# Performance work log

Measured on AMD Instinct MI355X. Metric: run time of the kernel, lower is better.

The kernel has to match this reference:

```python
import jax, jax.numpy as jnp
import numpy as np

N, E, D = 20000, 160000, 128   # nodes, edges, d_model
GH, HC = 4, 128                # TransformerConv heads, per-head channels (= out_channels)
MH = 4                         # temporal MHA heads
MC = D // MH                   # temporal MHA per-head dim
EPS = 1e-5


def layer_norm(x, g, b):
    mu = x.mean(-1, keepdims=True)
    var = ((x - mu) ** 2).mean(-1, keepdims=True)
    return (x - mu) * jax.lax.rsqrt(var + EPS) * g + b


def forward(x, temporal_encoding, gq_w, gq_b, gk_w, gk_b, gv_w, gv_b, gs_w, gs_b,
            mha_wq, mha_bq, mha_wk, mha_bk, mha_wv, mha_bv, mha_wo, mha_bo,
            ffn_w1, ffn_b1, ffn_w2, ffn_b2,
            ln1_g, ln1_b, ln2_g, ln2_b, ln3_g, ln3_b, edge_index):
    src, dst = edge_index[0], edge_index[1]
    n = x.shape[0]
    # --- TransformerConv(in=D, out=D, heads=GH, concat=False, root_weight=True) ---
    q = (x @ gq_w.T + gq_b).reshape(n, GH, HC)
    k = (x @ gk_w.T + gk_b).reshape(n, GH, HC)
    v = (x @ gv_w.T + gv_b).reshape(n, GH, HC)
    # per-edge attention logits: <q_i, k_j> / sqrt(out_channels), message j->i
    alpha = (q[dst] * k[src]).sum(-1) / jnp.sqrt(jnp.asarray(HC, x.dtype))  # [E, GH]
    # numerically-stable segment softmax over incoming edges of each dst node
    m = jax.ops.segment_max(alpha, dst, num_segments=n)                     # [N, GH]
    ex = jnp.exp(alpha - m[dst])
    den = jax.ops.segment_sum(ex, dst, num_segments=n)
    w = ex / den[dst]                                                       # [E, GH]
    agg = jax.ops.segment_sum(w[..., None] * v[src], dst, num_segments=n)  # [N, GH, HC]
    graph_out = agg.mean(1) + (x @ gs_w.T + gs_b)  # concat=False -> head mean; + root skip lin
    x1 = layer_norm(x + graph_out, ln1_g, ln1_b)   # dropout is identity at eval
    # --- temporal MHA: per-node query (len 1) attends to its temporal encoding (kv len 1) ---
    tq = (x1 @ mha_wq.T + mha_bq).reshape(n, MH, MC)
    tk = (temporal_encoding @ mha_wk.T + mha_bk).reshape(n, MH, MC)
    tv = (temporal_encoding @ mha_wv.T + mha_bv).reshape(n, MH, MC)
    scores = (tq * tk).sum(-1, keepdims=True) / jnp.sqrt(jnp.asarray(MC, x.dtype))  # [N, MH, 1]
    attn = jax.nn.softmax(scores, axis=-1)  # exactly ones (single kv position); kept for fidelity
    temp_out = (attn * tv).reshape(n, D) @ mha_wo.T + mha_bo
    x2 = layer_norm(x1 + temp_out, ln2_g, ln2_b)
    # --- FFN ---
    h = jax.nn.relu(x2 @ ffn_w1.T + ffn_b1)
    ffn_out = h @ ffn_w2.T + ffn_b2
    return layer_norm(x2 + ffn_out, ln3_g, ln3_b)


def setup_inputs() -> dict:
    ks = jax.random.split(jax.random.key(0), 16)
    s = 0.05
    def p(i, shape):
        return jax.random.normal(ks[i], shape, jnp.float32) * s
    z = lambda *sh: jnp.zeros(sh, jnp.float32)
    o = lambda *sh: jnp.ones(sh, jnp.float32)
    return {
        "x": p(0, (N, D)),
        "temporal_encoding": p(1, (N, D)),
        "gq_w": p(2, (GH * HC, D)), "gq_b": z(GH * HC),
        "gk_w": p(3, (GH * HC, D)), "gk_b": z(GH * HC),
        "gv_w": p(4, (GH * HC, D)), "gv_b": z(GH * HC),
        "gs_w": p(5, (D, D)), "gs_b": z(D),
        "mha_wq": p(6, (D, D)), "mha_bq": z(D),
        "mha_wk": p(7, (D, D)), "mha_bk": z(D),
        "mha_wv": p(8, (D, D)), "mha_bv": z(D),
        "mha_wo": p(9, (D, D)), "mha_bo": z(D),
        "ffn_w1": p(10, (4 * D, D)), "ffn_b1": z(4 * D),
        "ffn_w2": p(11, (D, 4 * D)), "ffn_b2": z(D),
        "ln1_g": o(D), "ln1_b": z(D),
        "ln2_g": o(D), "ln2_b": z(D),
        "ln3_g": o(D), "ln3_b": z(D),
        "edge_index": jax.random.randint(ks[12], (2, E), 0, N, jnp.int32),
    }


def reference(x, temporal_encoding, gq_w, gq_b, gk_w, gk_b, gv_w, gv_b, gs_w, gs_b,
              mha_wq, mha_bq, mha_wk, mha_bk, mha_wv, mha_bv, mha_wo, mha_bo,
              ffn_w1, ffn_b1, ffn_w2, ffn_b2,
              ln1_g, ln1_b, ln2_g, ln2_b, ln3_g, ln3_b, edge_index):
    return forward(x, temporal_encoding, gq_w, gq_b, gk_w, gk_b, gv_w, gv_b, gs_w, gs_b,
                   mha_wq, mha_bq, mha_wk, mha_bk, mha_wv, mha_bv, mha_wo, mha_bo,
                   ffn_w1, ffn_b1, ffn_w2, ffn_b2,
                   ln1_g, ln1_b, ln2_g, ln2_b, ln3_g, ln3_b, edge_index)
```

## Files before the change

kernel.cpp:

```cpp
#include <hip/hip_runtime.h>

#define NN 20000
#define EE 160000
#define DD 128
#define GHC 512
#define INV_SQRT_HC 0.08838834764831845f

typedef __attribute__((ext_vector_type(8))) short short8;
typedef __attribute__((ext_vector_type(4))) short short4v;
typedef __attribute__((ext_vector_type(4))) float float4v;
typedef __attribute__((ext_vector_type(2))) float float2v;
typedef __attribute__((ext_vector_type(4))) unsigned uint4v;
typedef __attribute__((ext_vector_type(2))) unsigned uint2v;

__device__ inline float bf2f(unsigned short u) {
    union { unsigned u; float f; } x; x.u = ((unsigned)u) << 16; return x.f;
}
__device__ inline unsigned short f2bf(float f) {
    union { float f; unsigned u; } x; x.f = f;
    unsigned u = x.u;
    unsigned r = (u + 0x7fffu + ((u >> 16) & 1u)) >> 16;
    return (unsigned short)r;
}
__device__ inline unsigned cvt_pk_bf16(float a, float b) {
    unsigned d;
    asm("v_cvt_pk_bf16_f32 %0, %1, %2" : "=v"(d) : "v"(a), "v"(b));
    return d;
}

__device__ inline void stage16(const short8* gsrc, short8* ldst) {
    __builtin_amdgcn_global_load_lds(
        (const __attribute__((address_space(1))) void*)gsrc,
        (__attribute__((address_space(3))) void*)ldst, 16, 0, 0);
}

#if defined(__has_builtin)
#if __has_builtin(__builtin_amdgcn_cvt_pk_f32_fp8) && __has_builtin(__builtin_amdgcn_cvt_pk_fp8_f32)
#define HW_FP8 1
#endif
#endif
#ifndef HW_FP8
#define HW_FP8 0
#endif

#if !HW_FP8
__device__ inline unsigned char sw_enc_fp8(float f) {
    if (!(f == f)) return 0x7f;
    unsigned s = (f < 0.f) ? 0x80u : 0u;
    float a = fabsf(f);
    if (a >= 448.f) return (unsigned char)(s | 0x7e);
    if (a < 5.96046448e-8f) return (unsigned char)s;
    int e; frexpf(a, &e);
    int E = e - 1;
    if (E < -6) E = -6;
    float q = ldexpf(rintf(ldexpf(a, 3 - E)), E - 3);
    if (q == 0.f) return (unsigned char)s;
    union { float f; unsigned u; } x; x.f = q;
    int qe = (int)((x.u >> 23) & 0xff) - 127;
    if (qe < -6) {
        unsigned mant = (unsigned)rintf(ldexpf(q, 9));
        return (unsigned char)(s | mant);
    }
    unsigned mant = (x.u >> 20) & 7;
    int ebits = qe + 7;
    if (ebits > 15) { ebits = 15; mant = 6; }
    return (unsigned char)(s | ((unsigned)ebits << 3) | mant);
}
__device__ inline float sw_dec_fp8(unsigned char u) {
    unsigned s = u >> 7, e = (u >> 3) & 15, m = u & 7;
    float v = e ? ldexpf((float)(8 + m), (int)e - 10) : ldexpf((float)m, -9);
    return s ? -v : v;
}
#endif

__device__ inline unsigned fp8_enc4(float a, float b, float c, float d) {
#if HW_FP8
    int r = __builtin_amdgcn_cvt_pk_fp8_f32(a, b, 0, false);
    r = __builtin_amdgcn_cvt_pk_fp8_f32(c, d, r, true);
    return (unsigned)r;
#else
    return (unsigned)sw_enc_fp8(a) | ((unsigned)sw_enc_fp8(b) << 8)
         | ((unsigned)sw_enc_fp8(c) << 16) | ((unsigned)sw_enc_fp8(d) << 24);
#endif
}
__device__ inline float2v fp8_dec2_lo(unsigned w) {
#if HW_FP8
    return __builtin_amdgcn_cvt_pk_f32_fp8((int)w, false);
#else
    float2v r;
    r[0] = sw_dec_fp8((unsigned char)(w & 0xff));
    r[1] = sw_dec_fp8((unsigned char)((w >> 8) & 0xff));
    return r;
#endif
}
__device__ inline float2v fp8_dec2_hi(unsigned w) {
#if HW_FP8
    return __builtin_amdgcn_cvt_pk_f32_fp8((int)w, true);
#else
    float2v r;
    r[0] = sw_dec_fp8((unsigned char)((w >> 16) & 0xff));
    r[1] = sw_dec_fp8((unsigned char)(w >> 24));
    return r;
#endif
}

struct WPack { const void* in[18]; };
__device__ __constant__ const int WSZ[18] = {
    65536, 65536, 65536, 512, 512, 512,
    16384, 128, 65536, 512, 65536, 128,
    128, 128, 128, 128, 128, 128 };

__global__ void prep_kernel(const float* __restrict__ x, const float* __restrict__ te,
                            unsigned short* __restrict__ xcout, WPack p,
                            unsigned short* __restrict__ wcout,
                            const float* __restrict__ wv, const float* __restrict__ bv,
                            const float* __restrict__ wo, const float* __restrict__ bo,
                            unsigned short* __restrict__ wcomb,
                            unsigned short* __restrict__ bcomb,
                            const int* __restrict__ e_dst, int* __restrict__ counts)
{
    const int b = blockIdx.x;
    const int tid = threadIdx.x;
    if (b < 1024) {
        const long n4half = (long)NN * DD / 4;
        short4v* out4 = reinterpret_cast<short4v*>(xcout);
        long i = (long)b * 256 + tid;
        const long stride = 1024L * 256;
        const long tot = 2 * n4half;
        for (; i < tot; i += stride) {
            const float4v* src = (i < n4half)
                ? reinterpret_cast<const float4v*>(x)
                : reinterpret_cast<const float4v*>(te) - n4half;
            float4v v = src[i];
            short4v o;
            o[0] = (short)f2bf(v[0]); o[1] = (short)f2bf(v[1]);
            o[2] = (short)f2bf(v[2]); o[3] = (short)f2bf(v[3]);
            out4[i] = o;
        }
    } else if (b < 1600) {
        const int seg = (b - 1024) >> 5;
        const int rep = (b - 1024) & 31;
        int off = 0;
#pragma unroll
        for (int s = 0; s < 18; ++s) if (s < seg) off += WSZ[s];
        const int n = WSZ[seg];
        const float* q = (const float*)p.in[seg];
        for (int i = rep * 256 + tid; i < n; i += 32 * 256)
            wcout[off + i] = f2bf(q[i]);
    } else if (b < 1664) {
        int e = (b - 1600) * 256 + tid;
        int i = e >> 7, kk = e & 127;
        float s = 0.f;
        for (int j = 0; j < 128; ++j)
            s += wo[i * 128 + j] * wv[j * 128 + kk];
        wcomb[e] = f2bf(s);
        if (b == 1600 && tid < 128) {
            float t = 0.f;
            for (int j = 0; j < 128; ++j) t += wo[tid * 128 + j] * bv[j];
            bcomb[tid] = f2bf(t + bo[tid]);
        }
    } else {
        int e = (b - 1664) * 256 + tid;
        if (e < EE) {
            int d = e_dst[e];
            if (d >= 0 && d < NN) atomicAdd(&counts[d], 1);
        }
    }
}

__global__ __launch_bounds__(256) void gemm3_kernel(
    const unsigned short* __restrict__ A, const unsigned short* __restrict__ W,
    const unsigned short* __restrict__ bias, unsigned short* __restrict__ out,
    unsigned char* __restrict__ kvout, int M, int Nout, int split, int relu,
    int nxg, int ncol)
{
    __shared__ short8 wslab[2048];
    __shared__ __attribute__((aligned(16))) unsigned stile4[4][16][32];
    const int tid  = threadIdx.x;
    const int lane = tid & 63;
    const int wid  = tid >> 6;
    const int quad = lane >> 4;
    const int l15  = lane & 15;

    const int nb  = nxg * ncol;
    const int qq  = nb >> 3, rm = nb & 7;
    const int xcd = blockIdx.x & 7, slot = blockIdx.x >> 3;
    const int c   = (xcd < rm) ? xcd * (qq + 1) + slot
                               : rm * (qq + 1) + (xcd - rm) * qq + slot;
    const int xg = c / ncol;
    const int yg = c - xg * ncol;
    const int colbase0 = yg * 128;
    const int rowg = xg * 256;

    const bool isfp8 = (colbase0 >= split);
    const int kvcol = colbase0 - split;
    const int which = isfp8 ? (kvcol >> 9) : 0;
    const int head  = isfp8 ? ((kvcol & 511) >> 7) : 0;

    const short8* A8 = reinterpret_cast<const short8*>(A);
    const short8* W8 = reinterpret_cast<const short8*>(W);

    short8 a4[4];
    {
        int arow = rowg + wid * 16 + l15;
        if (arow >= M) arow = M - 1;
#pragma unroll
        for (int i = 0; i < 4; ++i) a4[i] = A8[(size_t)arow * 16 + i * 4 + quad];
    }

#pragma unroll
    for (int rep = 0; rep < 8; ++rep) {
        const int fi  = (rep * 4 + wid) & 3;
        const int ft  = rep & 3;
        const int ftt = rep >> 2;
        const int wrow = colbase0 + ftt * 64 + 16 * ft + l15;
        stage16(&W8[(size_t)wrow * 16 + fi * 4 + quad], &wslab[rep * 256 + wid * 64]);
    }

    short4v bs4[2][4];
#pragma unroll
    for (int tt = 0; tt < 2; ++tt)
#pragma unroll
        for (int t = 0; t < 4; ++t)
            bs4[tt][t] = *reinterpret_cast<const short4v*>(
                &bias[colbase0 + tt * 64 + 16 * t + quad * 4]);

    __syncthreads();

    unsigned* fpd = &stile4[wid][0][0];

#pragma unroll
    for (int tg = 0; tg < 4; ++tg) {
        const int rowbase = rowg + tg * 64 + wid * 16;

        short8 a4n[4];
        if (tg < 3) {
            int arow = rowbase + 64 + l15;
            if (arow >= M) arow = M - 1;
#pragma unroll
            for (int i = 0; i < 4; ++i) a4n[i] = A8[(size_t)arow * 16 + i * 4 + quad];
        }

#pragma unroll
        for (int tt = 0; tt < 2; ++tt) {
            float4v acc[4];
#pragma unroll
            for (int t = 0; t < 4; ++t) acc[t] = (float4v){0.f, 0.f, 0.f, 0.f};

#pragma unroll
            for (int i = 0; i < 4; ++i) {
#pragma unroll
                for (int t = 0; t < 4; ++t) {
                    short8 wb = wslab[((tt * 4 + t) * 4 + i) * 64 + lane];
                    acc[t] = __builtin_amdgcn_mfma_f32_16x16x32_bf16(wb, a4[i], acc[t], 0, 0, 0);
                }
            }

            if (!isfp8) {
#pragma unroll
                for (int t = 0; t < 4; ++t) {
                    float v0 = acc[t][0] + bf2f((unsigned short)bs4[tt][t][0]);
                    float v1 = acc[t][1] + bf2f((unsigned short)bs4[tt][t][1]);
                    float v2 = acc[t][2] + bf2f((unsigned short)bs4[tt][t][2]);
                    float v3 = acc[t][3] + bf2f((unsigned short)bs4[tt][t][3]);
                    if (relu) {
                        v0 = fmaxf(v0, 0.f); v1 = fmaxf(v1, 0.f);
                        v2 = fmaxf(v2, 0.f); v3 = fmaxf(v3, 0.f);
                    }
                    uint2v d = { cvt_pk_bf16(v0, v1), cvt_pk_bf16(v2, v3) };
                    const int dc = (8 * t + quad * 2) ^ ((l15 & 7) << 2);
                    *reinterpret_cast<uint2v*>(&stile4[wid][l15][dc]) = d;
                }
                const int rr0 = lane >> 3;
                const int cd  = (lane & 7) * 4;
#pragma unroll
                for (int it = 0; it < 2; ++it) {
                    int rw = rr0 + it * 8;
                    int grow = rowbase + rw;
                    if (grow < M) {
                        const int cs = cd ^ ((rw & 7) << 2);
                        uint4v v = *reinterpret_cast<const uint4v*>(&stile4[wid][rw][cs]);
                        *reinterpret_cast<uint4v*>(&out[(size_t)grow * Nout + colbase0 + tt * 64 + cd * 2]) = v;
                    }
                }
            } else {
#pragma unroll
                for (int t = 0; t < 4; ++t) {
                    float v0 = (acc[t][0] + bf2f((unsigned short)bs4[tt][t][0])) * 256.f;
                    float v1 = (acc[t][1] + bf2f((unsigned short)bs4[tt][t][1])) * 256.f;
                    float v2 = (acc[t][2] + bf2f((unsigned short)bs4[tt][t][2])) * 256.f;
                    float v3 = (acc[t][3] + bf2f((unsigned short)bs4[tt][t][3])) * 256.f;
                    const int dc = (tt * 16 + 4 * t + quad) ^ ((l15 & 7) << 2);
                    fpd[l15 * 32 + dc] = fp8_enc4(v0, v1, v2, v3);
                }
            }
        }

        if (isfp8) {
#pragma unroll
            for (int it = 0; it < 2; ++it) {
                int u = lane + it * 64;
                int row = u >> 3;
                int part = u & 7;
                int grow = rowbase + row;
                if (grow < M) {
                    const int db = row * 32 + ((part * 4) ^ ((row & 7) << 2));
                    uint4v v = *reinterpret_cast<const uint4v*>(&fpd[db]);
                    size_t ro = (size_t)grow * 1024 + (size_t)which * 512
                              + (size_t)head * 128 + (size_t)part * 16;
                    *reinterpret_cast<uint4v*>(kvout + ro) = v;
                }
            }
        }

        if (tg < 3) {
#pragma unroll
            for (int i = 0; i < 4; ++i) a4[i] = a4n[i];
        }
    }
}

__global__ __launch_bounds__(256) void gemm_ffn_ln_kernel(
    const unsigned short* __restrict__ A,
    const unsigned short* __restrict__ W1,
    const unsigned short* __restrict__ b1,
    const unsigned short* __restrict__ W2,
    const unsigned short* __restrict__ b2,
    const float* __restrict__ residf,
    const unsigned short* __restrict__ g, const unsigned short* __restrict__ beta,
    float* __restrict__ outf, int M)
{
    __shared__ short8 wslab[2048];
    __shared__ __attribute__((aligned(16))) unsigned short htile[64 * 128];
    const int tid  = threadIdx.x;
    const int lane = tid & 63;
    const int wid  = tid >> 6;
    const int quad = lane >> 4;
    const int l15  = lane & 15;
    const int rowbase = blockIdx.x * 64 + wid * 16;
    const int grow = rowbase + l15;
    const int gr = (grow < M) ? grow : M - 1;
    const int hrow = wid * 16 + l15;
    char* hb = reinterpret_cast<char*>(htile);

    const short8* A8  = reinterpret_cast<const short8*>(A);
    const short8* W18 = reinterpret_cast<const short8*>(W1);
    const short8* W28 = reinterpret_cast<const short8*>(W2);

    short8 a4[4];
#pragma unroll
    for (int i = 0; i < 4; ++i) a4[i] = A8[(size_t)gr * 16 + i * 4 + quad];

    float4v acc2[2][4];
#pragma unroll
    for (int tt = 0; tt < 2; ++tt)
#pragma unroll
        for (int t = 0; t < 4; ++t) acc2[tt][t] = (float4v){0.f, 0.f, 0.f, 0.f};

    for (int cc = 0; cc < 4; ++cc) {
        __syncthreads();
#pragma unroll
        for (int rep = 0; rep < 8; ++rep) {
            const int fi  = (rep * 4 + wid) & 3;
            const int ft  = rep & 3;
            const int ftt = rep >> 2;
            const int wrow = cc * 128 + ftt * 64 + 16 * ft + l15;
            stage16(&W18[(size_t)wrow * 16 + fi * 4 + quad], &wslab[rep * 256 + wid * 64]);
        }
        __syncthreads();

        float4v acc1[2][4];
#pragma unroll
        for (int tt = 0; tt < 2; ++tt)
#pragma unroll
            for (int t = 0; t < 4; ++t) acc1[tt][t] = (float4v){0.f, 0.f, 0.f, 0.f};
#pragma unroll
        for (int tt = 0; tt < 2; ++tt)
#pragma unroll
            for (int i = 0; i < 4; ++i)
#pragma unroll
                for (int t = 0; t < 4; ++t) {
                    short8 wb = wslab[((tt * 4 + t) * 4 + i) * 64 + lane];
                    acc1[tt][t] = __builtin_amdgcn_mfma_f32_16x16x32_bf16(wb, a4[i], acc1[tt][t], 0, 0, 0);
                }
#pragma unroll
        for (int tt = 0; tt < 2; ++tt)
#pragma unroll
            for (int t = 0; t < 4; ++t) {
                const int n0 = tt * 64 + 16 * t + quad * 4;
                short4v bs = *reinterpret_cast<const short4v*>(&b1[cc * 128 + n0]);
                float v0 = fmaxf(acc1[tt][t][0] + bf2f((unsigned short)bs[0]), 0.f);
                float v1 = fmaxf(acc1[tt][t][1] + bf2f((unsigned short)bs[1]), 0.f);
                float v2 = fmaxf(acc1[tt][t][2] + bf2f((unsigned short)bs[2]), 0.f);
                float v3 = fmaxf(acc1[tt][t][3] + bf2f((unsigned short)bs[3]), 0.f);
                uint2v d = { cvt_pk_bf16(v0, v1), cvt_pk_bf16(v2, v3) };
                *reinterpret_cast<uint2v*>(
                    hb + ((hrow * 256 + n0 * 2) ^ ((hrow & 7) << 4))) = d;
            }

        __syncthreads();
#pragma unroll
        for (int rep = 0; rep < 8; ++rep) {
            const int fi  = (rep * 4 + wid) & 3;
            const int ft  = rep & 3;
            const int ftt = rep >> 2;
            const int wrow = ftt * 64 + 16 * ft + l15;
            stage16(&W28[(size_t)wrow * 64 + cc * 16 + fi * 4 + quad],
                    &wslab[rep * 256 + wid * 64]);
        }
        __syncthreads();

        short8 h4[4];
#pragma unroll
        for (int i = 0; i < 4; ++i)
            h4[i] = *reinterpret_cast<const short8*>(
                hb + ((hrow * 256 + (i * 32 + quad * 8) * 2) ^ ((hrow & 7) << 4)));
#pragma unroll
        for (int tt = 0; tt < 2; ++tt)
#pragma unroll
            for (int i = 0; i < 4; ++i)
#pragma unroll
                for (int t = 0; t < 4; ++t) {
                    short8 wb = wslab[((tt * 4 + t) * 4 + i) * 64 + lane];
                    acc2[tt][t] = __builtin_amdgcn_mfma_f32_16x16x32_bf16(wb, h4[i], acc2[tt][t], 0, 0, 0);
                }
    }

    float v[32];
#pragma unroll
    for (int tt = 0; tt < 2; ++tt)
#pragma unroll
        for (int t = 0; t < 4; ++t) {
            const int n0 = tt * 64 + 16 * t + quad * 4;
            short4v bs = *reinterpret_cast<const short4v*>(&b2[n0]);
            float4v rv = *reinterpret_cast<const float4v*>(&residf[(size_t)gr * 128 + n0]);
#pragma unroll
            for (int r = 0; r < 4; ++r)
                v[(tt * 4 + t) * 4 + r] = acc2[tt][t][r]
                    + bf2f((unsigned short)bs[r]) + rv[r];
        }
    float s = 0.f, sq = 0.f;
#pragma unroll
    for (int i = 0; i < 32; ++i) { s += v[i]; sq += v[i] * v[i]; }
    s  += __shfl_xor(s, 16, 64);  s  += __shfl_xor(s, 32, 64);
    sq += __shfl_xor(sq, 16, 64); sq += __shfl_xor(sq, 32, 64);
    float mu  = s * (1.f / 128.f);
    float var = sq * (1.f / 128.f) - mu * mu;
    float rs  = rsqrtf(fmaxf(var, 0.f) + 1e-5f);

    if (grow < M) {
#pragma unroll
        for (int tt = 0; tt < 2; ++tt)
#pragma unroll
            for (int t = 0; t < 4; ++t) {
                const int n0 = tt * 64 + 16 * t + quad * 4;
                short4v gg = *reinterpret_cast<const short4v*>(&g[n0]);
                short4v bb = *reinterpret_cast<const short4v*>(&beta[n0]);
                float4v ov;
#pragma unroll
                for (int r = 0; r < 4; ++r)
                    ov[r] = (v[(tt * 4 + t) * 4 + r] - mu) * rs
                            * bf2f((unsigned short)gg[r]) + bf2f((unsigned short)bb[r]);
                *reinterpret_cast<float4v*>(&outf[(size_t)grow * 128 + n0]) = ov;
            }
    }
}

__global__ __launch_bounds__(256) void gemm_ln12_kernel(
    const unsigned short* __restrict__ A1, const unsigned short* __restrict__ W1,
    const unsigned short* __restrict__ b1,
    const float* __restrict__ rx, const float* __restrict__ ragg,
    const unsigned short* __restrict__ g1, const unsigned short* __restrict__ be1,
    const unsigned short* __restrict__ A2, const unsigned short* __restrict__ W2,
    const unsigned short* __restrict__ b2,
    const unsigned short* __restrict__ g2, const unsigned short* __restrict__ be2,
    float* __restrict__ outf, unsigned short* __restrict__ outb, int M)
{
    __shared__ short8 wslab[2048];
    const int tid  = threadIdx.x;
    const int lane = tid & 63;
    const int wid  = tid >> 6;
    const int quad = lane >> 4;
    const int l15  = lane & 15;
    const int rowbase = blockIdx.x * 64 + wid * 16;

    const int grow = rowbase + l15;
    const int gr = (grow < M) ? grow : M - 1;

    const short8* A81 = reinterpret_cast<const short8*>(A1);
    const short8* A82 = reinterpret_cast<const short8*>(A2);
    const short8* W81 = reinterpret_cast<const short8*>(W1);
    const short8* W82 = reinterpret_cast<const short8*>(W2);

#pragma unroll
    for (int rep = 0; rep < 8; ++rep) {
        const int fi  = (rep * 4 + wid) & 3;
        const int ft  = rep & 3;
        const int ftt = rep >> 2;
        const int wrow = ftt * 64 + 16 * ft + l15;
        stage16(&W81[(size_t)wrow * 16 + fi * 4 + quad], &wslab[rep * 256 + wid * 64]);
    }
    short8 a4[4];
#pragma unroll
    for (int i = 0; i < 4; ++i) a4[i] = A81[(size_t)gr * 16 + i * 4 + quad];
    __syncthreads();

    float4v acc1[2][4];
#pragma unroll
    for (int tt = 0; tt < 2; ++tt)
#pragma unroll
        for (int t = 0; t < 4; ++t) acc1[tt][t] = (float4v){0.f, 0.f, 0.f, 0.f};
#pragma unroll
    for (int tt = 0; tt < 2; ++tt)
#pragma unroll
        for (int i = 0; i < 4; ++i)
#pragma unroll
            for (int t = 0; t < 4; ++t) {
                short8 wb = wslab[((tt * 4 + t) * 4 + i) * 64 + lane];
                acc1[tt][t] = __builtin_amdgcn_mfma_f32_16x16x32_bf16(wb, a4[i], acc1[tt][t], 0, 0, 0);
            }
    __syncthreads();

#pragma unroll
    for (int rep = 0; rep < 8; ++rep) {
        const int fi  = (rep * 4 + wid) & 3;
        const int ft  = rep & 3;
        const int ftt = rep >> 2;
        const int wrow = ftt * 64 + 16 * ft + l15;
        stage16(&W82[(size_t)wrow * 16 + fi * 4 + quad], &wslab[rep * 256 + wid * 64]);
    }
    short8 a42[4];
#pragma unroll
    for (int i = 0; i < 4; ++i) a42[i] = A82[(size_t)gr * 16 + i * 4 + quad];

    float x1[32];
    {
        float v[32];
#pragma unroll
        for (int tt = 0; tt < 2; ++tt)
#pragma unroll
            for (int t = 0; t < 4; ++t) {
                const int n0 = tt * 64 + 16 * t + quad * 4;
                short4v bs = *reinterpret_cast<const short4v*>(&b1[n0]);
                float4v rv = *reinterpret_cast<const float4v*>(&rx[(size_t)gr * 128 + n0]);
                float4v cv = *reinterpret_cast<const float4v*>(&ragg[(size_t)gr * 128 + n0]);
#pragma unroll
                for (int r = 0; r < 4; ++r)
                    v[(tt * 4 + t) * 4 + r] = acc1[tt][t][r]
                        + bf2f((unsigned short)bs[r]) + rv[r] + cv[r];
            }
        float s = 0.f, sq = 0.f;
#pragma unroll
        for (int i = 0; i < 32; ++i) { s += v[i]; sq += v[i] * v[i]; }
        s  += __shfl_xor(s, 16, 64);  s  += __shfl_xor(s, 32, 64);
        sq += __shfl_xor(sq, 16, 64); sq += __shfl_xor(sq, 32, 64);
        float mu  = s * (1.f / 128.f);
        float var = sq * (1.f / 128.f) - mu * mu;
        float rs  = rsqrtf(fmaxf(var, 0.f) + 1e-5f);
#pragma unroll
        for (int tt = 0; tt < 2; ++tt)
#pragma unroll
            for (int t = 0; t < 4; ++t) {
                const int n0 = tt * 64 + 16 * t + quad * 4;
                short4v gg = *reinterpret_cast<const short4v*>(&g1[n0]);
                short4v bb = *reinterpret_cast<const short4v*>(&be1[n0]);
#pragma unroll
                for (int r = 0; r < 4; ++r)
                    x1[(tt * 4 + t) * 4 + r] = (v[(tt * 4 + t) * 4 + r] - mu) * rs
                        * bf2f((unsigned short)gg[r]) + bf2f((unsigned short)bb[r]);
            }
    }

    __syncthreads();

    float4v acc2[2][4];
#pragma unroll
    for (int tt = 0; tt < 2; ++tt)
#pragma unroll
        for (int t = 0; t < 4; ++t) acc2[tt][t] = (float4v){0.f, 0.f, 0.f, 0.f};
#pragma unroll
    for (int tt = 0; tt < 2; ++tt)
#pragma unroll
        for (int i = 0; i < 4; ++i)
#pragma unroll
            for (int t = 0; t < 4; ++t) {
                short8 wb = wslab[((tt * 4 + t) * 4 + i) * 64 + lane];
                acc2[tt][t] = __builtin_amdgcn_mfma_f32_16x16x32_bf16(wb, a42[i], acc2[tt][t], 0, 0, 0);
            }

    float v[32];
#pragma unroll
    for (int tt = 0; tt < 2; ++tt)
#pragma unroll
        for (int t = 0; t < 4; ++t) {
            const int n0 = tt * 64 + 16 * t + quad * 4;
            short4v bs = *reinterpret_cast<const short4v*>(&b2[n0]);
#pragma unroll
            for (int r = 0; r < 4; ++r)
                v[(tt * 4 + t) * 4 + r] = acc2[tt][t][r]
                    + bf2f((unsigned short)bs[r]) + x1[(tt * 4 + t) * 4 + r];
        }
    float s = 0.f, sq = 0.f;
#pragma unroll
    for (int i = 0; i < 32; ++i) { s += v[i]; sq += v[i] * v[i]; }
    s  += __shfl_xor(s, 16, 64);  s  += __shfl_xor(s, 32, 64);
    sq += __shfl_xor(sq, 16, 64); sq += __shfl_xor(sq, 32, 64);
    float mu  = s * (1.f / 128.f);
    float var = sq * (1.f / 128.f) - mu * mu;
    float rs  = rsqrtf(fmaxf(var, 0.f) + 1e-5f);

    if (grow < M) {
#pragma unroll
        for (int tt = 0; tt < 2; ++tt)
#pragma unroll
            for (int t = 0; t < 4; ++t) {
                const int n0 = tt * 64 + 16 * t + quad * 4;
                short4v gg = *reinterpret_cast<const short4v*>(&g2[n0]);
                short4v bb = *reinterpret_cast<const short4v*>(&be2[n0]);
                float4v ov;
#pragma unroll
                for (int r = 0; r < 4; ++r)
                    ov[r] = (v[(tt * 4 + t) * 4 + r] - mu) * rs
                            * bf2f((unsigned short)gg[r]) + bf2f((unsigned short)bb[r]);
                *reinterpret_cast<float4v*>(&outf[(size_t)grow * 128 + n0]) = ov;
                uint2v d = { cvt_pk_bf16(ov[0], ov[1]), cvt_pk_bf16(ov[2], ov[3]) };
                *reinterpret_cast<uint2v*>(&outb[(size_t)grow * 128 + n0]) = d;
            }
    }
}

__global__ __launch_bounds__(1024) void scan_kernel(
    const int* __restrict__ counts, int* __restrict__ offsets, int* __restrict__ pos, int n)
{
    __shared__ int wsum[16];
    __shared__ int carry_s;
    const int tid = threadIdx.x;
    const int wid = tid >> 6, lane = tid & 63;
    int vals[20];
#pragma unroll
    for (int cI = 0; cI < 20; ++cI) {
        int i = cI * 1024 + tid;
        vals[cI] = (i < n) ? counts[i] : 0;
    }
    if (tid == 0) carry_s = 0;
    __syncthreads();
#pragma unroll
    for (int cI = 0; cI < 20; ++cI) {
        int i = cI * 1024 + tid;
        int val = vals[cI];
        int x = val;
#pragma unroll
        for (int off = 1; off < 64; off <<= 1) {
            int t = __shfl_up(x, off, 64);
            if (lane >= off) x += t;
        }
        if (lane == 63) wsum[wid] = x;
        __syncthreads();
        if (wid == 0 && lane < 16) {
            int s = wsum[lane];
#pragma unroll
            for (int off = 1; off < 16; off <<= 1) {
                int t = __shfl_up(s, off, 64);
                if (lane >= off) s += t;
            }
            wsum[lane] = s;
        }
        __syncthreads();
        int prefix = (wid > 0 ? wsum[wid - 1] : 0) + carry_s;
        int ex = prefix + x - val;
        if (i < n) { offsets[i] = ex; pos[i] = ex; }
        __syncthreads();
        if (tid == 0) carry_s += wsum[15];
        __syncthreads();
    }
    if (tid == 0) offsets[n] = carry_s;
}

__global__ void scatter_kernel(const int* __restrict__ src, const int* __restrict__ dst,
                               int* __restrict__ pos, int* __restrict__ sorted_src, int E)
{
    int e = blockIdx.x * 256 + threadIdx.x;
    if (e < E) {
        int d = dst[e];
        if (d >= 0 && d < NN) {
            int p = atomicAdd(&pos[d], 1);
            if (p >= 0 && p < E) sorted_src[p] = src[e];
        }
    }
}

__device__ inline void agg_edge(const uint2v& kk, const uint2v& vv,
                                const float* qf, float* acc, float& ssum)
{
    float2v k01 = fp8_dec2_lo(kk[0]);
    float2v k23 = fp8_dec2_hi(kk[0]);
    float2v k45 = fp8_dec2_lo(kk[1]);
    float2v k67 = fp8_dec2_hi(kk[1]);
    float dot = qf[0] * k01[0] + qf[1] * k01[1] + qf[2] * k23[0] + qf[3] * k23[1]
              + qf[4] * k45[0] + qf[5] * k45[1] + qf[6] * k67[0] + qf[7] * k67[1];
    dot += __shfl_xor(dot, 1, 64);
    dot += __shfl_xor(dot, 2, 64);
    dot += __shfl_xor(dot, 4, 64);
    dot += __shfl_xor(dot, 8, 64);
    float pp = __expf(dot);
    ssum += pp;
    float2v v01 = fp8_dec2_lo(vv[0]);
    float2v v23 = fp8_dec2_hi(vv[0]);
    float2v v45 = fp8_dec2_lo(vv[1]);
    float2v v67 = fp8_dec2_hi(vv[1]);
    acc[0] += pp * v01[0]; acc[1] += pp * v01[1];
    acc[2] += pp * v23[0]; acc[3] += pp * v23[1];
    acc[4] += pp * v45[0]; acc[5] += pp * v45[1];
    acc[6] += pp * v67[0]; acc[7] += pp * v67[1];
}

__global__ __launch_bounds__(256) void agg_kernel(
    const unsigned short* __restrict__ q, const unsigned char* __restrict__ kvb,
    const int* __restrict__ offsets, const int* __restrict__ srcs,
    float* __restrict__ aggb)
{
    __shared__ float sacc[4][64][8];
    __shared__ float sssum[4][64];
    const int tid  = threadIdx.x;
    const int wid  = tid >> 6;
    const int lane = tid & 63;
    const int node = blockIdx.x * 2 + (wid >> 1);
    const int half = wid & 1;

    const short8* q8 = reinterpret_cast<const short8*>(q);
    const int fidx = (lane >> 4) * 16 + (lane & 15);
    const int koff = fidx * 8;

    short8 qv = q8[(size_t)node * 64 + fidx];
    float qf[8];
#pragma unroll
    for (int i = 0; i < 8; ++i)
        qf[i] = bf2f((unsigned short)qv[i]) * (INV_SQRT_HC / 256.f);

    int beg = offsets[node], end = offsets[node + 1];
    if (beg < 0) beg = 0;
    if (end > EE) end = EE;
    float ssum = 0.f;
    float acc[8];
#pragma unroll
    for (int i = 0; i < 8; ++i) acc[i] = 0.f;

    const int start = beg + half;
    int nce = (end > start) ? ((end - start + 1) >> 1) : 0;
    int ncap = (nce > 64) ? 64 : nce;

    int sv = 0;
    if (lane < ncap) {
        int s = srcs[start + 2 * lane];
        if (s < 0) s = 0;
        if (s >= NN) s = NN - 1;
        sv = s;
    }
    if (ncap > 0) {
        int s0 = __shfl(sv, 0, 64);
        uint2v kc = *reinterpret_cast<const uint2v*>(kvb + (size_t)s0 * 1024 + koff);
        uint2v vc = *reinterpret_cast<const uint2v*>(kvb + (size_t)s0 * 1024 + 512 + koff);
        for (int i = 0; i < ncap; ++i) {
            uint2v kn, vn;
            if (i + 1 < ncap) {
                int sn = __shfl(sv, i + 1, 64);
                kn = *reinterpret_cast<const uint2v*>(kvb + (size_t)sn * 1024 + koff);
                vn = *reinterpret_cast<const uint2v*>(kvb + (size_t)sn * 1024 + 512 + koff);
            }
            agg_edge(kc, vc, qf, acc, ssum);
            kc = kn; vc = vn;
        }
    }
    for (int j = start + 128; j < end; j += 2) {
        int s = srcs[j];
        if (s < 0) s = 0;
        if (s >= NN) s = NN - 1;
        uint2v kc = *reinterpret_cast<const uint2v*>(kvb + (size_t)s * 1024 + koff);
        uint2v vc = *reinterpret_cast<const uint2v*>(kvb + (size_t)s * 1024 + 512 + koff);
        agg_edge(kc, vc, qf, acc, ssum);
    }

#pragma unroll
    for (int i = 0; i < 8; ++i) sacc[wid][lane][i] = acc[i];
    sssum[wid][lane] = ssum;
    __syncthreads();
    if (half == 0) {
#pragma unroll
        for (int i = 0; i < 8; ++i) acc[i] += sacc[wid ^ 1][lane][i];
        ssum += sssum[wid ^ 1][lane];

        float inv = (ssum > 0.f) ? 1.f / (256.f * ssum) : 0.f;
#pragma unroll
        for (int i = 0; i < 8; ++i) acc[i] *= inv;
#pragma unroll
        for (int i = 0; i < 8; ++i) {
            acc[i] += __shfl_xor(acc[i], 16, 64);
            acc[i] += __shfl_xor(acc[i], 32, 64);
            acc[i] *= 0.25f;
        }
        if (lane < 16) {
            float4v* o = reinterpret_cast<float4v*>(aggb + (size_t)node * 128 + lane * 8);
            o[0] = (float4v){acc[0], acc[1], acc[2], acc[3]};
            o[1] = (float4v){acc[4], acc[5], acc[6], acc[7]};
        }
    }
}

extern "C" void kernel_launch(void* const* d_in, const int* in_sizes, int n_in,
                              void* d_out, int out_size, void* d_ws, size_t ws_size,
                              hipStream_t stream)
{
    const int* edge_index = (const int*)d_in[28];
    const int* e_src = edge_index;
    const int* e_dst = edge_index + EE;

    if (n_in < 29 || in_sizes[0] != NN * DD || in_sizes[28] != 2 * EE || out_size != NN * DD)
        return;

    const size_t SZ_OFF  = (size_t)(NN + 16) * 4;
    const size_t SZ_CNT  = (size_t)NN * 4;
    const size_t SZ_SS   = (size_t)EE * 4;
    const size_t SZ_SM   = (size_t)NN * DD * 2;
    const size_t SZ_F32  = (size_t)NN * DD * 4;
    const size_t SZ_Q    = (size_t)NN * 512 * 2;
    const size_t SZ_KV   = (size_t)NN * 1024;
    const size_t SZ_HB   = (size_t)NN * GHC * 2;
    const size_t WC_ELE  = 347136;
    const size_t SZ_WC   = WC_ELE * 2;
    const size_t SZ_WCB  = 16384 * 2 + 256;
    const size_t REQUIRED = SZ_OFF + 2 * SZ_CNT + SZ_SS + 2 * SZ_SM + SZ_WC + SZ_WCB
                          + SZ_Q + SZ_KV + 3 * SZ_F32 + SZ_SM + SZ_HB;

    if (ws_size < REQUIRED) return;

    char* w = (char*)d_ws;
    int* offsets = (int*)w;        w += SZ_OFF;
    int* counts  = (int*)w;        w += SZ_CNT;
    int* pos     = (int*)w;        w += SZ_CNT;
    int* sorted_src = (int*)w;     w += SZ_SS;
    unsigned short* xc   = (unsigned short*)w; w += SZ_SM;
    unsigned short* tec  = (unsigned short*)w; w += SZ_SM;
    unsigned short* wc   = (unsigned short*)w; w += SZ_WC;
    unsigned short* wcomb = (unsigned short*)w; w += 16384 * 2;
    unsigned short* bcomb = (unsigned short*)w; w += 256;
    unsigned short* qb   = (unsigned short*)w; w += SZ_Q;
    unsigned char*  kvb  = (unsigned char*)w;  w += SZ_KV;
    float*          aggb = (float*)w;          w += SZ_F32;
    float*          x1f  = (float*)w;          w += SZ_F32;
    float*          x2f  = (float*)w;          w += SZ_F32;
    unsigned short* x2b  = (unsigned short*)w; w += SZ_SM;
    unsigned short* hbuf = (unsigned short*)w; w += SZ_HB;
    (void)x1f; (void)hbuf;

    unsigned short* cw = wc;
    unsigned short* qkv_w = cw; cw += 3 * 65536;
    unsigned short* qkv_b = cw; cw += 3 * 512;
    unsigned short* gs_w  = cw; cw += 16384;  unsigned short* gs_b  = cw; cw += 128;
    unsigned short* ffn_w1 = cw; cw += 65536; unsigned short* ffn_b1 = cw; cw += 512;
    unsigned short* ffn_w2 = cw; cw += 65536; unsigned short* ffn_b2 = cw; cw += 128;
    unsigned short* ln1_g = cw; cw += 128;    unsigned short* ln1_b = cw; cw += 128;
    unsigned short* ln2_g = cw; cw += 128;    unsigned short* ln2_b = cw; cw += 128;
    unsigned short* ln3_g = cw; cw += 128;    unsigned short* ln3_b = cw; cw += 128;

    const int EB = (EE + 255) / 256;
    const dim3 blk(256);
    const int MB = (NN + 63) / 64;
    const int MB2 = (NN + 255) / 256;

    WPack pack;
    const int live_idx[18] = {2,4,6, 3,5,7, 8,9, 18,19, 20,21, 22,23,24,25,26,27};
    for (int i = 0; i < 18; ++i) pack.in[i] = d_in[live_idx[i]];

    (void)hipMemsetAsync(counts, 0, SZ_CNT, stream);
    prep_kernel<<<1664 + EB, blk, 0, stream>>>((const float*)d_in[0], (const float*)d_in[1],
                                               xc, pack, wc,
                                               (const float*)d_in[14], (const float*)d_in[15],
                                               (const float*)d_in[16], (const float*)d_in[17],
                                               wcomb, bcomb, e_dst, counts);

    scan_kernel<<<1, 1024, 0, stream>>>(counts, offsets, pos, NN);
    scatter_kernel<<<EB, blk, 0, stream>>>(e_src, e_dst, pos, sorted_src, EE);

    gemm3_kernel<<<dim3(MB2 * 12), blk, 0, stream>>>(xc, qkv_w, qkv_b, qb, kvb,
                                                     NN, 512, 512, 0, MB2, 12);
    agg_kernel<<<NN / 2, blk, 0, stream>>>(qb, kvb, offsets, sorted_src, aggb);
    gemm_ln12_kernel<<<MB, blk, 0, stream>>>(xc, gs_w, gs_b,
                                             (const float*)d_in[0], aggb,
                                             ln1_g, ln1_b,
                                             tec, wcomb, bcomb,
                                             ln2_g, ln2_b, x2f, x2b, NN);
    gemm_ffn_ln_kernel<<<MB, blk, 0, stream>>>(x2b, ffn_w1, ffn_b1, ffn_w2, ffn_b2,
                                               x2f, ln3_g, ln3_b, (float*)d_out, NN);
}
```

Measured before the change: 262.7 us.

## Halve QKV GEMM column tile and batch four edge gathers in aggregation

The QKV projection GEMM now uses 64-column tiles instead of 128, which doubles the grid to 24 column groups and halves the weight slab in LDS. This is meant to raise occupancy and spread the work more evenly across CUs, at the cost of re-reading each A row twice as often. The fp8 K/V epilogue is reworked with a new swizzle and a half-head offset to fit the narrower tile. Separately, the aggregation loop now issues four edge K/V gathers before computing, replacing one-ahead prefetching, to expose more memory-level parallelism.

```diff
diff --git a/kernel.cpp b/kernel.cpp
--- a/kernel.cpp
+++ b/kernel.cpp
@@ -174,7 +174,7 @@
     unsigned char* __restrict__ kvout, int M, int Nout, int split, int relu,
     int nxg, int ncol)
 {
-    __shared__ short8 wslab[2048];
+    __shared__ short8 wslab[1024];
     __shared__ __attribute__((aligned(16))) unsigned stile4[4][16][32];
     const int tid  = threadIdx.x;
     const int lane = tid & 63;
@@ -189,13 +189,14 @@
                                : rm * (qq + 1) + (xcd - rm) * qq + slot;
     const int xg = c / ncol;
     const int yg = c - xg * ncol;
-    const int colbase0 = yg * 128;
+    const int colbase0 = yg * 64;
     const int rowg = xg * 256;
 
     const bool isfp8 = (colbase0 >= split);
     const int kvcol = colbase0 - split;
     const int which = isfp8 ? (kvcol >> 9) : 0;
-    const int head  = isfp8 ? ((kvcol & 511) >> 7) : 0;
+    const int head  = isfp8 ? ((kvcol >> 7) & 3) : 0;
+    const int halfh = isfp8 ? ((kvcol >> 6) & 1) : 0;
 
     const short8* A8 = reinterpret_cast<const short8*>(A);
     const short8* W8 = reinterpret_cast<const short8*>(W);
@@ -209,21 +210,16 @@
     }
 
 #pragma unroll
-    for (int rep = 0; rep < 8; ++rep) {
-        const int fi  = (rep * 4 + wid) & 3;
-        const int ft  = rep & 3;
-        const int ftt = rep >> 2;
-        const int wrow = colbase0 + ftt * 64 + 16 * ft + l15;
-        stage16(&W8[(size_t)wrow * 16 + fi * 4 + quad], &wslab[rep * 256 + wid * 64]);
-    }
-
-    short4v bs4[2][4];
-#pragma unroll
-    for (int tt = 0; tt < 2; ++tt)
-#pragma unroll
-        for (int t = 0; t < 4; ++t)
-            bs4[tt][t] = *reinterpret_cast<const short4v*>(
-                &bias[colbase0 + tt * 64 + 16 * t + quad * 4]);
+    for (int rep = 0; rep < 4; ++rep) {
+        const int wrow = colbase0 + rep * 16 + l15;
+        stage16(&W8[(size_t)wrow * 16 + wid * 4 + quad], &wslab[rep * 256 + wid * 64]);
+    }
+
+    short4v bs4[4];
+#pragma unroll
+    for (int t = 0; t < 4; ++t)
+        bs4[t] = *reinterpret_cast<const short4v*>(
+            &bias[colbase0 + t * 16 + quad * 4]);
 
     __syncthreads();
 
@@ -241,62 +237,33 @@
             for (int i = 0; i < 4; ++i) a4n[i] = A8[(size_t)arow * 16 + i * 4 + quad];
         }
 
-#pragma unroll
-        for (int tt = 0; tt < 2; ++tt) {
-            float4v acc[4];
-#pragma unroll
-            for (int t = 0; t < 4; ++t) acc[t] = (float4v){0.f, 0.f, 0.f, 0.f};
-
-#pragma unroll
-            for (int i = 0; i < 4; ++i) {
-#pragma unroll
-                for (int t = 0; t < 4; ++t) {
-                    short8 wb = wslab[((tt * 4 + t) * 4 + i) * 64 + lane];
-                    acc[t] = __builtin_amdgcn_mfma_f32_16x16x32_bf16(wb, a4[i], acc[t], 0, 0, 0);
+        float4v acc[4];
+#pragma unroll
+        for (int t = 0; t < 4; ++t) acc[t] = (float4v){0.f, 0.f, 0.f, 0.f};
+#pragma unroll
+        for (int i = 0; i < 4; ++i) {
+#pragma unroll
+            for (int t = 0; t < 4; ++t) {
+                short8 wb = wslab[t * 256 + i * 64 + lane];
+                acc[t] = __builtin_amdgcn_mfma_f32_16x16x32_bf16(wb, a4[i], acc[t], 0, 0, 0);
+            }
+        }
+
+        if (!isfp8) {
+#pragma unroll
+            for (int t = 0; t < 4; ++t) {
+                float v0 = acc[t][0] + bf2f((unsigned short)bs4[t][0]);
+                float v1 = acc[t][1] + bf2f((unsigned short)bs4[t][1]);
+                float v2 = acc[t][2] + bf2f((unsigned short)bs4[t][2]);
+                float v3 = acc[t][3] + bf2f((unsigned short)bs4[t][3]);
+                if (relu) {
+                    v0 = fmaxf(v0, 0.f); v1 = fmaxf(v1, 0.f);
+                    v2 = fmaxf(v2, 0.f); v3 = fmaxf(v3, 0.f);
                 }
-            }
-
-            if (!isfp8) {
-#pragma unroll
-                for (int t = 0; t < 4; ++t) {
-                    float v0 = acc[t][0] + bf2f((unsigned short)bs4[tt][t][0]);
-                    float v1 = acc[t][1] + bf2f((unsigned short)bs4[tt][t][1]);
-                    float v2 = acc[t][2] + bf2f((unsigned short)bs4[tt][t][2]);
-                    float v3 = acc[t][3] + bf2f((unsigned short)bs4[tt][t][3]);
-                    if (relu) {
-                        v0 = fmaxf(v0, 0.f); v1 = fmaxf(v1, 0.f);
-                        v2 = fmaxf(v2, 0.f); v3 = fmaxf(v3, 0.f);
-                    }
-                    uint2v d = { cvt_pk_bf16(v0, v1), cvt_pk_bf16(v2, v3) };
-                    const int dc = (8 * t + quad * 2) ^ ((l15 & 7) << 2);
-                    *reinterpret_cast<uint2v*>(&stile4[wid][l15][dc]) = d;
-                }
-                const int rr0 = lane >> 3;
-                const int cd  = (lane & 7) * 4;
-#pragma unroll
-                for (int it = 0; it < 2; ++it) {
-                    int rw = rr0 + it * 8;
-                    int grow = rowbase + rw;
-                    if (grow < M) {
-                        const int cs = cd ^ ((rw & 7) << 2);
-                        uint4v v = *reinterpret_cast<const uint4v*>(&stile4[wid][rw][cs]);
-                        *reinterpret_cast<uint4v*>(&out[(size_t)grow * Nout + colbase0 + tt * 64 + cd * 2]) = v;
-                    }
-                }
-            } else {
-#pragma unroll
-                for (int t = 0; t < 4; ++t) {
-                    float v0 = (acc[t][0] + bf2f((unsigned short)bs4[tt][t][0])) * 256.f;
-                    float v1 = (acc[t][1] + bf2f((unsigned short)bs4[tt][t][1])) * 256.f;
-                    float v2 = (acc[t][2] + bf2f((unsigned short)bs4[tt][t][2])) * 256.f;
-                    float v3 = (acc[t][3] + bf2f((unsigned short)bs4[tt][t][3])) * 256.f;
-                    const int dc = (tt * 16 + 4 * t + quad) ^ ((l15 & 7) << 2);
-                    fpd[l15 * 32 + dc] = fp8_enc4(v0, v1, v2, v3);
-                }
-            }
-        }
-
-        if (isfp8) {
+                uint2v d = { cvt_pk_bf16(v0, v1), cvt_pk_bf16(v2, v3) };
+                const int dc = (t * 8 + quad * 2) ^ ((l15 & 7) << 2);
+                *reinterpret_cast<uint2v*>(&stile4[wid][l15][dc]) = d;
+            }
 #pragma unroll
             for (int it = 0; it < 2; ++it) {
                 int u = lane + it * 64;
@@ -304,10 +271,31 @@
                 int part = u & 7;
                 int grow = rowbase + row;
                 if (grow < M) {
-                    const int db = row * 32 + ((part * 4) ^ ((row & 7) << 2));
+                    const int cs = (part * 4) ^ ((row & 7) << 2);
+                    uint4v v = *reinterpret_cast<const uint4v*>(&stile4[wid][row][cs]);
+                    *reinterpret_cast<uint4v*>(&out[(size_t)grow * Nout + colbase0 + part * 8]) = v;
+                }
+            }
+        } else {
+#pragma unroll
+            for (int t = 0; t < 4; ++t) {
+                float v0 = (acc[t][0] + bf2f((unsigned short)bs4[t][0])) * 256.f;
+                float v1 = (acc[t][1] + bf2f((unsigned short)bs4[t][1])) * 256.f;
+                float v2 = (acc[t][2] + bf2f((unsigned short)bs4[t][2])) * 256.f;
+                float v3 = (acc[t][3] + bf2f((unsigned short)bs4[t][3])) * 256.f;
+                const int dc = (t * 4 + quad) ^ (((l15 >> 1) & 3) << 2);
+                fpd[l15 * 16 + dc] = fp8_enc4(v0, v1, v2, v3);
+            }
+            {
+                int row = lane >> 2;
+                int part = lane & 3;
+                int grow = rowbase + row;
+                if (grow < M) {
+                    const int db = row * 16 + ((part ^ ((row >> 1) & 3)) << 2);
                     uint4v v = *reinterpret_cast<const uint4v*>(&fpd[db]);
                     size_t ro = (size_t)grow * 1024 + (size_t)which * 512
-                              + (size_t)head * 128 + (size_t)part * 16;
+                              + (size_t)head * 128 + (size_t)halfh * 64
+                              + (size_t)part * 16;
                     *reinterpret_cast<uint4v*>(kvout + ro) = v;
                 }
             }
@@ -756,20 +744,37 @@
         if (s >= NN) s = NN - 1;
         sv = s;
     }
-    if (ncap > 0) {
-        int s0 = __shfl(sv, 0, 64);
-        uint2v kc = *reinterpret_cast<const uint2v*>(kvb + (size_t)s0 * 1024 + koff);
-        uint2v vc = *reinterpret_cast<const uint2v*>(kvb + (size_t)s0 * 1024 + 512 + koff);
-        for (int i = 0; i < ncap; ++i) {
-            uint2v kn, vn;
-            if (i + 1 < ncap) {
-                int sn = __shfl(sv, i + 1, 64);
-                kn = *reinterpret_cast<const uint2v*>(kvb + (size_t)sn * 1024 + koff);
-                vn = *reinterpret_cast<const uint2v*>(kvb + (size_t)sn * 1024 + 512 + koff);
-            }
-            agg_edge(kc, vc, qf, acc, ssum);
-            kc = kn; vc = vn;
-        }
+    for (int base = 0; base < ncap; base += 4) {
+        const int rem = ncap - base;
+        uint2v k0{}, v0{}, k1{}, v1{}, k2{}, v2{}, k3{}, v3{};
+        {
+            int s = __shfl(sv, base, 64);
+            const unsigned char* p = kvb + (size_t)s * 1024 + koff;
+            k0 = *reinterpret_cast<const uint2v*>(p);
+            v0 = *reinterpret_cast<const uint2v*>(p + 512);
+        }
+        if (rem > 1) {
+            int s = __shfl(sv, base + 1, 64);
+            const unsigned char* p = kvb + (size_t)s * 1024 + koff;
+            k1 = *reinterpret_cast<const uint2v*>(p);
+            v1 = *reinterpret_cast<const uint2v*>(p + 512);
+        }
+        if (rem > 2) {
+            int s = __shfl(sv, base + 2, 64);
+            const unsigned char* p = kvb + (size_t)s * 1024 + koff;
+            k2 = *reinterpret_cast<const uint2v*>(p);
+            v2 = *reinterpret_cast<const uint2v*>(p + 512);
+        }
+        if (rem > 3) {
+            int s = __shfl(sv, base + 3, 64);
+            const unsigned char* p = kvb + (size_t)s * 1024 + koff;
+            k3 = *reinterpret_cast<const uint2v*>(p);
+            v3 = *reinterpret_cast<const uint2v*>(p + 512);
+        }
+        agg_edge(k0, v0, qf, acc, ssum);
+        if (rem > 1) agg_edge(k1, v1, qf, acc, ssum);
+        if (rem > 2) agg_edge(k2, v2, qf, acc, ssum);
+        if (rem > 3) agg_edge(k3, v3, qf, acc, ssum);
     }
     for (int j = start + 128; j < end; j += 2) {
         int s = srcs[j];
@@ -881,8 +886,8 @@
     scan_kernel<<<1, 1024, 0, stream>>>(counts, offsets, pos, NN);
     scatter_kernel<<<EB, blk, 0, stream>>>(e_src, e_dst, pos, sorted_src, EE);
 
-    gemm3_kernel<<<dim3(MB2 * 12), blk, 0, stream>>>(xc, qkv_w, qkv_b, qb, kvb,
-                                                     NN, 512, 512, 0, MB2, 12);
+    gemm3_kernel<<<dim3(MB2 * 24), blk, 0, stream>>>(xc, qkv_w, qkv_b, qb, kvb,
+                                                     NN, 512, 512, 0, MB2, 24);
     agg_kernel<<<NN / 2, blk, 0, stream>>>(qb, kvb, offsets, sorted_src, aggb);
     gemm_ln12_kernel<<<MB, blk, 0, stream>>>(xc, gs_w, gs_b,
                                              (const float*)d_in[0], aggb,
```

Result: no change. 261.1 us (-0.6%).
